# Kernel tuning notes

Hardware: AMD Instinct MI355X
Metric: run time of the kernel (lower is better)

Reference implementation:

```python
import jax, jax.numpy as jnp
import numpy as np

GRID = 128  # voxel grid extent
N_PTS = 100000


def _hash(c):
    c = c.astype(np.int64) + 16  # shift so offset-perturbed coords stay non-negative
    return (c[:, 0] * 512 + c[:, 1]) * 512 + c[:, 2]


def _offsets(vals):
    v = np.asarray(vals)
    return np.stack(np.meshgrid(v, v, v, indexing='ij'), axis=-1).reshape(-1, 3)


def _build_kmap(cin, cout, offsets):
    # For each kernel offset o, find pairs (in_idx, out_idx) with coord_in == coord_out + o.
    ki = _hash(cin)
    order = np.argsort(ki)
    ks = ki[order]
    ins, outs = [], []
    for o in offsets:
        q = _hash(cout + o[None, :])
        pos = np.searchsorted(ks, q)
        pc = np.clip(pos, 0, len(ks) - 1)
        found = ks[pc] == q
        ins.append(order[pc[found]])
        outs.append(np.nonzero(found)[0])
    K = len(offsets)
    P = max(1, max(len(a) for a in ins))
    in_idx = np.full((K, P), len(cin), np.int32)   # pad -> zero row of padded feats
    out_idx = np.full((K, P), len(cout), np.int32)  # pad -> dummy output row
    for k in range(K):
        in_idx[k, :len(ins[k])] = ins[k]
        out_idx[k, :len(outs[k])] = outs[k]
    return in_idx, out_idx


def _conv(x, W, in_idx, out_idx, n_out):
    # Minkowski sparse conv: per kernel offset, gather -> matmul -> scatter-add.
    xp = jnp.concatenate([x, jnp.zeros((1, x.shape[1]), x.dtype)], axis=0)
    out0 = jnp.zeros((n_out + 1, W.shape[-1]), x.dtype)

    def step(acc, kio):
        Wk, ik, ok = kio
        return acc.at[ok].add(xp[ik] @ Wk), None

    out, _ = jax.lax.scan(step, out0, (W, in_idx, out_idx))
    return out[:n_out]


def _bn(x, gamma, beta, eps=1e-5):
    # training-mode batch norm over the point dimension (biased variance)
    m = jnp.mean(x, axis=0)
    v = jnp.mean((x - m) ** 2, axis=0)
    return (x - m) * jax.lax.rsqrt(v + eps) * gamma + beta


def _forward(feats, W0, g0, b0,
             Ws1, gs1, bs1, Wa1, ga1, ba1, Wb1, gb1, bb1,
             Ws2, gs2, bs2, Wa2, ga2, ba2, Wb2, gb2, bb2, Wd2, gd2, bd2,
             Ws3, gs3, bs3, Wa3, ga3, ba3, Wb3, gb3, bb3, Wd3, gd3, bd3,
             c1, c2, c3,
             im0, om0, ims1, oms1, imb1, omb1, ims2, oms2, imb2, omb2,
             ims3, oms3, imb3, omb3):
    relu = jax.nn.relu
    n0, n1, n2, n3 = feats.shape[0], c1.shape[0], c2.shape[0], c3.shape[0]
    # stem: 5x5x5 conv + BN + ReLU (output coords == input coords)
    x = relu(_bn(_conv(feats, W0, im0, om0, n0), g0, b0))
    # level 1: stride-2 conv + BN + ReLU, then BasicBlock 64->64 (identity residual)
    x = relu(_bn(_conv(x, Ws1, ims1, oms1, n1), gs1, bs1))
    h = relu(_bn(_conv(x, Wa1, imb1, omb1, n1), ga1, ba1))
    h = _bn(_conv(h, Wb1, imb1, omb1, n1), gb1, bb1)
    y1 = relu(h + x)
    # level 2: stride-2 conv, then BasicBlock 64->128 (1x1 conv + BN residual)
    x = relu(_bn(_conv(y1, Ws2, ims2, oms2, n2), gs2, bs2))
    res = _bn(x @ Wd2, gd2, bd2)
    h = relu(_bn(_conv(x, Wa2, imb2, omb2, n2), ga2, ba2))
    h = _bn(_conv(h, Wb2, imb2, omb2, n2), gb2, bb2)
    y2 = relu(h + res)
    # level 3: stride-2 conv, then BasicBlock 128->256 (1x1 conv + BN residual)
    x = relu(_bn(_conv(y2, Ws3, ims3, oms3, n3), gs3, bs3))
    res = _bn(x @ Wd3, gd3, bd3)
    h = relu(_bn(_conv(x, Wa3, imb3, omb3, n3), ga3, ba3))
    h = _bn(_conv(h, Wb3, imb3, omb3, n3), gb3, bb3)
    y3 = relu(h + res)
    return (y1, y2, y3)


def setup_inputs() -> dict:
    rng = np.random.default_rng(0)
    c0 = np.unique(rng.integers(0, GRID, size=(N_PTS, 3)), axis=0).astype(np.int32)
    c1 = np.unique(c0 // 2 * 2, axis=0)
    c2 = np.unique(c1 // 4 * 4, axis=0)
    c3 = np.unique(c2 // 8 * 8, axis=0)
    im0, om0 = _build_kmap(c0, c0, _offsets([-2, -1, 0, 1, 2]))  # conv0 k=5, ts=1
    ims1, oms1 = _build_kmap(c0, c1, _offsets([0, 1]))           # stride-2, ts_in=1
    imb1, omb1 = _build_kmap(c1, c1, _offsets([-2, 0, 2]))       # k=3 at ts=2
    ims2, oms2 = _build_kmap(c1, c2, _offsets([0, 2]))
    imb2, omb2 = _build_kmap(c2, c2, _offsets([-4, 0, 4]))       # k=3 at ts=4
    ims3, oms3 = _build_kmap(c2, c3, _offsets([0, 4]))
    imb3, omb3 = _build_kmap(c3, c3, _offsets([-8, 0, 8]))       # k=3 at ts=8
    keys = iter(jax.random.split(jax.random.key(0), 16))

    def kai3(K, ci, co):  # kaiming_normal fan_out for [K, Cin, Cout] sparse kernels
        return jax.random.normal(next(keys), (K, ci, co), jnp.float32) * np.float32(np.sqrt(2.0 / (K * co)))

    def kai2(ci, co):
        return jax.random.normal(next(keys), (ci, co), jnp.float32) * np.float32(np.sqrt(2.0 / co))

    ones = lambda c: jnp.ones((c,), jnp.float32)
    zeros = lambda c: jnp.zeros((c,), jnp.float32)
    feats = jax.random.normal(next(keys), (c0.shape[0], 1), jnp.float32)
    return dict(
        feats=feats,
        W0=kai3(125, 1, 64), g0=ones(64), b0=zeros(64),
        Ws1=kai3(8, 64, 64), gs1=ones(64), bs1=zeros(64),
        Wa1=kai3(27, 64, 64), ga1=ones(64), ba1=zeros(64),
        Wb1=kai3(27, 64, 64), gb1=ones(64), bb1=zeros(64),
        Ws2=kai3(8, 64, 64), gs2=ones(64), bs2=zeros(64),
        Wa2=kai3(27, 64, 128), ga2=ones(128), ba2=zeros(128),
        Wb2=kai3(27, 128, 128), gb2=ones(128), bb2=zeros(128),
        Wd2=kai2(64, 128), gd2=ones(128), bd2=zeros(128),
        Ws3=kai3(8, 128, 128), gs3=ones(128), bs3=zeros(128),
        Wa3=kai3(27, 128, 256), ga3=ones(256), ba3=zeros(256),
        Wb3=kai3(27, 256, 256), gb3=ones(256), bb3=zeros(256),
        Wd3=kai2(128, 256), gd3=ones(256), bd3=zeros(256),
        c1=jnp.asarray(c1), c2=jnp.asarray(c2), c3=jnp.asarray(c3),
        im0=jnp.asarray(im0), om0=jnp.asarray(om0),
        ims1=jnp.asarray(ims1), oms1=jnp.asarray(oms1),
        imb1=jnp.asarray(imb1), omb1=jnp.asarray(omb1),
        ims2=jnp.asarray(ims2), oms2=jnp.asarray(oms2),
        imb2=jnp.asarray(imb2), omb2=jnp.asarray(omb2),
        ims3=jnp.asarray(ims3), oms3=jnp.asarray(oms3),
        imb3=jnp.asarray(imb3), omb3=jnp.asarray(omb3),
    )


def reference(feats, W0, g0, b0,
              Ws1, gs1, bs1, Wa1, ga1, ba1, Wb1, gb1, bb1,
              Ws2, gs2, bs2, Wa2, ga2, ba2, Wb2, gb2, bb2, Wd2, gd2, bd2,
              Ws3, gs3, bs3, Wa3, ga3, ba3, Wb3, gb3, bb3, Wd3, gd3, bd3,
              c1, c2, c3,
              im0, om0, ims1, oms1, imb1, omb1, ims2, oms2, imb2, omb2,
              ims3, oms3, imb3, omb3):
    return _forward(feats, W0, g0, b0,
                    Ws1, gs1, bs1, Wa1, ga1, ba1, Wb1, gb1, bb1,
                    Ws2, gs2, bs2, Wa2, ga2, ba2, Wb2, gb2, bb2, Wd2, gd2, bd2,
                    Ws3, gs3, bs3, Wa3, ga3, ba3, Wb3, gb3, bb3, Wd3, gd3, bd3,
                    c1, c2, c3,
                    im0, om0, ims1, oms1, imb1, omb1, ims2, oms2, imb2, omb2,
                    ims3, oms3, imb3, omb3)
```

## Files before the change

kernel.cpp:

```cpp
#include <hip/hip_runtime.h>
#include <hip/hip_bf16.h>
#include <cstdint>
#include <cstddef>

typedef __attribute__((ext_vector_type(8))) short sh8;
typedef __attribute__((ext_vector_type(4))) short sh4;
typedef __attribute__((ext_vector_type(4))) int ix4;
typedef __attribute__((ext_vector_type(16))) float floatx16;
typedef unsigned short ushort_t;

__device__ __forceinline__ void glds16(const ushort_t* g, ushort_t* l) {
  __builtin_amdgcn_global_load_lds(
      (const __attribute__((address_space(1))) void*)g,
      (__attribute__((address_space(3))) void*)l, 16, 0, 0);
}

__device__ __forceinline__ ushort_t f2bf_bits(float f) {
  __hip_bfloat16 b = __float2bfloat16(f);
  return __builtin_bit_cast(unsigned short, b);
}
__device__ __forceinline__ float bf2f(ushort_t u) {
  unsigned int x = ((unsigned int)u) << 16;
  return __builtin_bit_cast(float, x);
}

__global__ void build_ell_kernel(const int* __restrict__ in_idx,
                                 const int* __restrict__ out_idx,
                                 int K, int S, int P, int n_in, int n_out,
                                 int* __restrict__ ell) {
  int i = blockIdx.x * 256 + threadIdx.x;
  if (i >= K * P) return;
  int vin = in_idx[i];
  int vout = out_idx[i];
  if (vin < n_in && vout < n_out) {
    ell[(size_t)vout * S + (i / P)] = vin;
  }
}

__global__ void pack_u_kernel(const float* __restrict__ W,
                              __hip_bfloat16* __restrict__ Wp,
                              int K, int CSPLIT, int COUT, long total) {
  long i = (long)blockIdx.x * 256 + threadIdx.x;
  if (i >= total) return;
  int co = (int)(i % COUT);
  long t = i / COUT;
  int vch = (int)(t % 64);
  int vk = (int)(t / 64);
  int k = vk / CSPLIT;
  int ci = (vk % CSPLIT) * 64 + vch;
  int CIN = CSPLIT * 64;
  float v = (k < K) ? W[((long)k * CIN + ci) * COUT + co] : 0.f;
  Wp[(((long)vk * 8 + (vch >> 3)) * COUT + co) * 8 + (vch & 7)] =
      __float2bfloat16(v);
}

__global__ void pack_w0_kernel(const float* __restrict__ W,
                               __hip_bfloat16* __restrict__ Wp) {
  int i = blockIdx.x * 256 + threadIdx.x;
  if (i >= 128 * 64) return;
  int co = i & 63;
  int ki = i >> 6;
  float v = (ki < 125) ? W[ki * 64 + co] : 0.f;
  Wp[(((ki >> 4) * 64) + co) * 16 + (ki & 15)] = __float2bfloat16(v);
}

__global__ void f2bf_kernel(const float* __restrict__ x,
                            __hip_bfloat16* __restrict__ y, long n, long npad) {
  long i = (long)blockIdx.x * 256 + threadIdx.x;
  if (i >= npad) return;
  y[i] = __float2bfloat16(i < n ? x[i] : 0.f);
}

__global__ void reduce_parts_kernel(const ushort_t* __restrict__ part, int P,
                                    long total, ushort_t* __restrict__ out) {
  long i = (long)blockIdx.x * 256 + threadIdx.x;
  if (i >= total) return;
  float s = 0.f;
  for (int p = 0; p < P; ++p) s += bf2f(part[(size_t)p * total + i]);
  out[i] = f2bf_bits(s);
}

__global__ __launch_bounds__(256, 2) void conv0_mfma_kernel(
    const ushort_t* __restrict__ xpad, const ushort_t* __restrict__ Wp0,
    const int* __restrict__ ell, int n_out, ushort_t* __restrict__ out) {
  constexpr int STR = 152;
  __shared__ ushort_t xs[64 * STR];
  const int tid = threadIdx.x;
  const int lane = tid & 63;
  const int wv = tid >> 6;
  const int wm = wv & 1, wn = wv >> 1;
  const long m0 = (long)blockIdx.x * 64;
  const int row = tid >> 2;
  const int kk0 = (tid & 3) * 32;
  const long grow = m0 + row;

  if (grow < n_out) {
    const ix4* ep = (const ix4*)(ell + grow * 128 + kk0);
#pragma unroll
    for (int g = 0; g < 8; ++g) {
      ix4 e = ep[g];
      sh4 v;
#pragma unroll
      for (int j = 0; j < 4; ++j) {
        int ix = (e[j] < 0) ? n_out : e[j];
        v[j] = (short)xpad[ix];
      }
      *(sh4*)(&xs[row * STR + kk0 + g * 4]) = v;
    }
  } else {
    sh4 z = (sh4)(short)0;
#pragma unroll
    for (int g = 0; g < 8; ++g) *(sh4*)(&xs[row * STR + kk0 + g * 4]) = z;
  }
  __syncthreads();

  const int arow = wm * 32 + (lane & 31);
  const int koff = (lane >> 5) * 8;
  const int bcol = wn * 32 + (lane & 31);
  floatx16 acc = (floatx16)(0.0f);
#pragma unroll
  for (int kc = 0; kc < 8; ++kc) {
    sh8 a = *(const sh8*)(&xs[arow * STR + kc * 16 + koff]);
    sh8 b = *(const sh8*)(Wp0 + ((size_t)kc * 64 + bcol) * 16 + koff);
    acc = __builtin_amdgcn_mfma_f32_32x32x16_bf16(a, b, acc, 0, 0, 0);
  }
  const int lrow = (lane >> 5) * 4;
#pragma unroll
  for (int r = 0; r < 16; ++r) {
    long orow = m0 + wm * 32 + (r & 3) + 8 * (r >> 2) + lrow;
    if (orow < n_out) out[orow * 64 + bcol] = f2bf_bits(acc[r]);
  }
}

template <int CSPLIT, int CT, bool HASELL>
__global__ __launch_bounds__(CT * 4, CT == 128 ? 4 : 3) void conv_u_kernel(
    const ushort_t* __restrict__ xb, const ushort_t* __restrict__ Wp,
    const int* __restrict__ ell, int S, int KI, int KP, int kdense,
    int n_out, int n_in, int COfull, int MB, int KS, int CS,
    ushort_t* __restrict__ out) {
  constexpr int BLK = CT * 4;
  constexpr int NWN = CT / 32;
  constexpr int ASEG_PW = 16 / (BLK / 64);
  constexpr int BSEG_PW = (CT / 8) / (BLK / 64);
  constexpr int RW = CSPLIT * 64;
  __shared__ ushort_t Ab[2][128 * 64];
  __shared__ ushort_t Bb[2][8 * CT * 8];
  const int tid = threadIdx.x;
  const int lane = tid & 63;
  const int wv = tid >> 6;
  const int wm = wv / NWN, wn = wv % NWN;

  const int total = MB * KS * CS;
  const int l = blockIdx.x;
  const int q = total >> 3, r8 = total & 7;
  const int xcd = l & 7, pos = l >> 3;
  const int lp = (xcd < r8) ? (xcd * (q + 1) + pos)
                            : (r8 * (q + 1) + (xcd - r8) * q + pos);
  const int mblk = lp / (KS * CS);
  const int rem = lp - mblk * (KS * CS);
  const int yk = rem / CS;
  const int zc = rem - yk * CS;
  const long m0 = (long)mblk * 128;
  const int colbase = zc * CT;

  const int i0 = yk * KP;
  int cnt = KI - i0;
  if (cnt > KP) cnt = KP;
  out += (size_t)yk * ((size_t)n_out * COfull);

  floatx16 acc0 = (floatx16)(0.0f);
  floatx16 acc1 = (floatx16)(0.0f);

  auto loadEll = [&](int vk, int (&e)[ASEG_PW]) {
    if constexpr (HASELL) {
      const int kq = (CSPLIT == 1) ? vk : (vk / CSPLIT);
#pragma unroll
      for (int i = 0; i < ASEG_PW; ++i) {
        const int s = wv * ASEG_PW + i;
        const int r = s * 8 + (lane >> 3);
        long grow = m0 + r;
        long gc = grow < (long)(n_out - 1) ? grow : (long)(n_out - 1);
        e[i] = ell[gc * (long)S + kq];
      }
    }
  };

  auto stage = [&](int vk, ushort_t* A, ushort_t* B, int (&eRaw)[ASEG_PW]) {
    const int sub = (CSPLIT == 1) ? 0 : (vk % CSPLIT);
    const int kq = (CSPLIT == 1) ? vk : (vk / CSPLIT);
#pragma unroll
    for (int i = 0; i < ASEG_PW; ++i) {
      const int s = wv * ASEG_PW + i;
      const int r = s * 8 + (lane >> 3);
      const long grow = m0 + r;
      int v;
      if constexpr (HASELL) v = eRaw[i];
      else v = (kq < kdense) ? (int)grow : -1;
      if (grow >= (long)n_out) v = -1;
      const int e = (v < 0) ? n_in : v;
      const int c = lane & 7;
      const int lc = c ^ (r & 7);
      glds16(xb + (size_t)e * RW + sub * 64 + lc * 8, A + s * 512 + lane * 8);
    }
    const ushort_t* wb = Wp + (size_t)vk * 8 * COfull * 8;
#pragma unroll
    for (int i = 0; i < BSEG_PW; ++i) {
      const int s = wv * BSEG_PW + i;
      int lc, co;
      if (CT == 128) { lc = s >> 1; co = (s & 1) * 64 + lane; }
      else           { lc = s;      co = lane; }
      glds16(wb + ((size_t)lc * COfull + colbase + co) * 8,
             B + s * 512 + lane * 8);
    }
  };
  auto compute = [&](const ushort_t* A, const ushort_t* B) {
    const int r0 = wm * 64 + (lane & 31);
    const int h = lane >> 5;
    const int co = wn * 32 + (lane & 31);
#pragma unroll
    for (int kc = 0; kc < 4; ++kc) {
      const int lc = kc * 2 + h;
      const int pc = lc ^ (r0 & 7);
      sh8 a0 = *(const sh8*)(A + r0 * 64 + pc * 8);
      sh8 a1 = *(const sh8*)(A + (r0 + 32) * 64 + pc * 8);
      sh8 b = *(const sh8*)(B + ((size_t)lc * CT + co) * 8);
      acc0 = __builtin_amdgcn_mfma_f32_32x32x16_bf16(a0, b, acc0, 0, 0, 0);
      acc1 = __builtin_amdgcn_mfma_f32_32x32x16_bf16(a1, b, acc1, 0, 0, 0);
    }
  };

  constexpr int NWAIT = (ASEG_PW + BSEG_PW) + (HASELL ? ASEG_PW : 0);

  int eE[ASEG_PW] = {}, eO[ASEG_PW] = {};
  loadEll(i0, eE);
  stage(i0, Ab[0], Bb[0], eE);
  if (cnt > 1) loadEll(i0 + 1, eO);

#define CONV_ITER(J, P, SE, SO)                                                \
  if ((J) < cnt) {                                                             \
    __builtin_amdgcn_sched_barrier(0);             \
    asm volatile("s_waitcnt lgkmcnt(0)" ::: "memory");                         \
    __builtin_amdgcn_s_barrier();        \
    if ((J) + 1 < cnt) {                                                       \
      stage(i0 + (J) + 1, Ab[(P) ^ 1], Bb[(P) ^ 1], SO);                       \
      if ((J) + 2 < cnt) loadEll(i0 + (J) + 2, SE);                            \
      if constexpr (NWAIT == 4)                                                \
        asm volatile("s_waitcnt vmcnt(4)" ::: "memory");                       \
      else if constexpr (NWAIT == 6)                                           \
        asm volatile("s_waitcnt vmcnt(6)" ::: "memory");                       \
      else                                                                     \
        asm volatile("s_waitcnt vmcnt(10)" ::: "memory");                      \
    } else {                                                                   \
      asm volatile("s_waitcnt vmcnt(0)" ::: "memory");                         \
    }                                                                          \
    __builtin_amdgcn_s_barrier();           \
    __builtin_amdgcn_sched_barrier(0);                                         \
    compute(Ab[P], Bb[P]);                                                     \
  }

  for (int j = 0; j < cnt; j += 2) {
    CONV_ITER(j, 0, eE, eO)
    CONV_ITER(j + 1, 1, eO, eE)
  }
#undef CONV_ITER

  const int ccol = colbase + wn * 32 + (lane & 31);
  const int rb = wm * 64 + (lane >> 5) * 4;
#pragma unroll
  for (int rr = 0; rr < 16; ++rr) {
    long row = m0 + rb + (rr & 3) + 8 * (rr >> 2);
    if (row < n_out) out[row * COfull + ccol] = f2bf_bits(acc0[rr]);
    long row1 = row + 32;
    if (row1 < n_out) out[row1 * COfull + ccol] = f2bf_bits(acc1[rr]);
  }
}

template <int C>
__global__ void bn_reduce1_kernel(const ushort_t* __restrict__ x, int n,
                                  float* __restrict__ part) {
  constexpr int C4 = C / 4;
  constexpr int RL = 256 / C4;
  const int c4 = threadIdx.x % C4;
  const int rl = threadIdx.x / C4;
  float4 s = {0.f, 0.f, 0.f, 0.f}, ss = {0.f, 0.f, 0.f, 0.f};
  for (long row = (long)blockIdx.x * RL + rl; row < n;
       row += (long)gridDim.x * RL) {
    ushort4 u = *(const ushort4*)(x + row * C + c4 * 4);
    float v0 = bf2f(u.x), v1 = bf2f(u.y), v2 = bf2f(u.z), v3 = bf2f(u.w);
    s.x += v0; s.y += v1; s.z += v2; s.w += v3;
    ss.x += v0 * v0; ss.y += v1 * v1; ss.z += v2 * v2; ss.w += v3 * v3;
  }
  __shared__ float4 sh[512];
  sh[threadIdx.x] = s;
  sh[256 + threadIdx.x] = ss;
  __syncthreads();
  if (rl == 0) {
#pragma unroll
    for (int j = 1; j < RL; ++j) {
      float4 a = sh[j * C4 + c4];
      float4 b = sh[256 + j * C4 + c4];
      s.x += a.x; s.y += a.y; s.z += a.z; s.w += a.w;
      ss.x += b.x; ss.y += b.y; ss.z += b.z; ss.w += b.w;
    }
    *(float4*)(part + (size_t)blockIdx.x * 2 * C + c4 * 4) = s;
    *(float4*)(part + (size_t)blockIdx.x * 2 * C + C + c4 * 4) = ss;
  }
}

template <int C>
__global__ void bn_reduce2_kernel(const float* __restrict__ part, int G,
                                  float* __restrict__ stats) {
  const int c = blockIdx.x;
  const int g = threadIdx.x;
  __shared__ float sh[512];
  float s = 0.f, ss = 0.f;
  if (g < G) {
    s = part[(size_t)g * 2 * C + c];
    ss = part[(size_t)g * 2 * C + C + c];
  }
  sh[g] = s;
  sh[256 + g] = ss;
  __syncthreads();
#pragma unroll
  for (int off = 128; off > 0; off >>= 1) {
    if (g < off) {
      sh[g] += sh[g + off];
      sh[256 + g] += sh[256 + g + off];
    }
    __syncthreads();
  }
  if (g == 0) {
    stats[c] = sh[0];
    stats[C + c] = sh[256];
  }
}

template <int C, bool RELU, bool RES, bool WF32>
__global__ void bn_apply_kernel(const ushort_t* __restrict__ x,
                                const float* __restrict__ stats,
                                const float* __restrict__ gamma,
                                const float* __restrict__ beta,
                                const float* __restrict__ res,
                                long total4, float inv_n,
                                float* __restrict__ out,
                                ushort_t* __restrict__ outb, long padEnd4) {
  constexpr int C4 = C / 4;
  for (long i = (long)blockIdx.x * 256 + threadIdx.x; i < padEnd4;
       i += (long)gridDim.x * 256) {
    if (i >= total4) {
      if (outb) *(ushort4*)(outb + i * 4) = (ushort4){0, 0, 0, 0};
      continue;
    }
    const int c4 = (int)(i % C4);
    float4 sum = *(const float4*)(stats + c4 * 4);
    float4 sq = *(const float4*)(stats + C + c4 * 4);
    float4 g4 = *(const float4*)(gamma + c4 * 4);
    float4 b4 = *(const float4*)(beta + c4 * 4);
    ushort4 u = *(const ushort4*)(x + i * 4);
    float vin[4] = {bf2f(u.x), bf2f(u.y), bf2f(u.z), bf2f(u.w)};
    float4 r4 = {0.f, 0.f, 0.f, 0.f};
    if (RES) r4 = *(const float4*)(res + i * 4);
    float o[4];
#pragma unroll
    for (int j = 0; j < 4; ++j) {
      float m = ((const float*)&sum)[j] * inv_n;
      float var = ((const float*)&sq)[j] * inv_n - m * m;
      float sc = rsqrtf(var + 1e-5f) * ((const float*)&g4)[j];
      float val = (vin[j] - m) * sc + ((const float*)&b4)[j];
      if (RES) val += ((const float*)&r4)[j];
      if (RELU) val = fmaxf(val, 0.f);
      o[j] = val;
    }
    if (WF32) *(float4*)(out + i * 4) = (float4){o[0], o[1], o[2], o[3]};
    if (outb) {
      ushort4 w = {f2bf_bits(o[0]), f2bf_bits(o[1]), f2bf_bits(o[2]),
                   f2bf_bits(o[3])};
      *(ushort4*)(outb + i * 4) = w;
    }
  }
}


extern "C" void kernel_launch(void* const* d_in, const int* in_sizes, int n_in,
                              void* d_out, int out_size, void* d_ws,
                              size_t ws_size, hipStream_t stream) {
  const float* feats = (const float*)d_in[0];
  const float* W0  = (const float*)d_in[1];
  const float* g0  = (const float*)d_in[2];
  const float* b0  = (const float*)d_in[3];
  const float* Ws1 = (const float*)d_in[4];
  const float* gs1 = (const float*)d_in[5];
  const float* bs1 = (const float*)d_in[6];
  const float* Wa1 = (const float*)d_in[7];
  const float* ga1 = (const float*)d_in[8];
  const float* ba1 = (const float*)d_in[9];
  const float* Wb1 = (const float*)d_in[10];
  const float* gb1 = (const float*)d_in[11];
  const float* bb1 = (const float*)d_in[12];
  const float* Ws2 = (const float*)d_in[13];
  const float* gs2 = (const float*)d_in[14];
  const float* bs2 = (const float*)d_in[15];
  const float* Wa2 = (const float*)d_in[16];
  const float* ga2 = (const float*)d_in[17];
  const float* ba2 = (const float*)d_in[18];
  const float* Wb2 = (const float*)d_in[19];
  const float* gb2 = (const float*)d_in[20];
  const float* bb2 = (const float*)d_in[21];
  const float* Wd2 = (const float*)d_in[22];
  const float* gd2 = (const float*)d_in[23];
  const float* bd2 = (const float*)d_in[24];
  const float* Ws3 = (const float*)d_in[25];
  const float* gs3 = (const float*)d_in[26];
  const float* bs3 = (const float*)d_in[27];
  const float* Wa3 = (const float*)d_in[28];
  const float* ga3 = (const float*)d_in[29];
  const float* ba3 = (const float*)d_in[30];
  const float* Wb3 = (const float*)d_in[31];
  const float* gb3 = (const float*)d_in[32];
  const float* bb3 = (const float*)d_in[33];
  const float* Wd3 = (const float*)d_in[34];
  const float* gd3 = (const float*)d_in[35];
  const float* bd3 = (const float*)d_in[36];
  const int* im0  = (const int*)d_in[40];
  const int* om0  = (const int*)d_in[41];
  const int* ims1 = (const int*)d_in[42];
  const int* oms1 = (const int*)d_in[43];
  const int* imb1 = (const int*)d_in[44];
  const int* omb1 = (const int*)d_in[45];
  const int* ims2 = (const int*)d_in[46];
  const int* oms2 = (const int*)d_in[47];
  const int* imb2 = (const int*)d_in[48];
  const int* omb2 = (const int*)d_in[49];
  const int* ims3 = (const int*)d_in[50];
  const int* oms3 = (const int*)d_in[51];
  const int* imb3 = (const int*)d_in[52];
  const int* omb3 = (const int*)d_in[53];

  const int n0 = in_sizes[0];
  const int n1 = in_sizes[37] / 3;
  const int n2 = in_sizes[38] / 3;
  const int n3 = in_sizes[39] / 3;
  const int P0  = in_sizes[40] / 125;
  const int Ps1 = in_sizes[42] / 8;
  const int Pb1 = in_sizes[44] / 27;
  const int Ps2 = in_sizes[46] / 8;
  const int Pb2 = in_sizes[48] / 27;
  const int Ps3 = in_sizes[50] / 8;
  const int Pb3 = in_sizes[52] / 27;

  char* w = (char*)d_ws;
  auto carve = [&](size_t bytes) {
    char* p = w;
    w += (bytes + 255) & ~(size_t)255;
    return p;
  };
  int* ellS = (int*)carve((size_t)n0 * 128 * sizeof(int));
  int* ellB = (int*)carve((size_t)n1 * 28 * sizeof(int));
  float* part = (float*)carve((size_t)256 * 512 * sizeof(float));
  float* stats = (float*)carve((size_t)512 * sizeof(float));
  size_t capE = (size_t)n0 * 64 + 512;
  float* buf1 = (float*)carve(capE * sizeof(float));
  float* buf2 = (float*)carve(capE * sizeof(float));
  __hip_bfloat16* bbA = (__hip_bfloat16*)carve(capE * 2);
  __hip_bfloat16* bbB = (__hip_bfloat16*)carve(capE * 2);
  __hip_bfloat16* bbC = (__hip_bfloat16*)carve(capE * 2);
  ushort_t* cb1 = (ushort_t*)carve(capE * 2);
  ushort_t* cb2 = (ushort_t*)carve(capE * 2);
  ushort_t* cb3 = (ushort_t*)carve(capE * 2);
  __hip_bfloat16* xfeat = (__hip_bfloat16*)carve(((size_t)n0 + 1) * 2);

  auto packu = [&](const float* W, int K, int cin, int cout) {
    int csplit = cin / 64;
    long tot = (long)K * csplit * 64 * cout;
    __hip_bfloat16* Wp = (__hip_bfloat16*)carve((size_t)tot * 2);
    pack_u_kernel<<<(int)((tot + 255) / 256), 256, 0, stream>>>(
        W, Wp, K, csplit, cout, tot);
    return Wp;
  };
  __hip_bfloat16* Wp0 = (__hip_bfloat16*)carve((size_t)128 * 64 * 2);
  pack_w0_kernel<<<32, 256, 0, stream>>>(W0, Wp0);
  __hip_bfloat16* Ps1p = packu(Ws1, 8, 64, 64);
  __hip_bfloat16* Pa1p = packu(Wa1, 27, 64, 64);
  __hip_bfloat16* Pb1p = packu(Wb1, 27, 64, 64);
  __hip_bfloat16* Ps2p = packu(Ws2, 8, 64, 64);
  __hip_bfloat16* Pd2p = packu(Wd2, 1, 64, 128);
  __hip_bfloat16* Pa2p = packu(Wa2, 27, 64, 128);
  __hip_bfloat16* Pb2p = packu(Wb2, 27, 128, 128);
  __hip_bfloat16* Ps3p = packu(Ws3, 8, 128, 128);
  __hip_bfloat16* Pd3p = packu(Wd3, 1, 128, 256);
  __hip_bfloat16* Pa3p = packu(Wa3, 27, 128, 256);
  __hip_bfloat16* Pb3p = packu(Wb3, 27, 256, 256);

  size_t used = (size_t)(w - (char*)d_ws);
  ushort_t* pbufU = (ushort_t*)w;
  size_t pcapU = (ws_size > used) ? (ws_size - used) / 2 : 0;

  f2bf_kernel<<<(int)((n0 + 256) / 256), 256, 0, stream>>>(feats, xfeat, n0,
                                                           n0 + 1);

  auto buildEll = [&](int* ellbuf, const int* im, const int* om, int K, int S,
                      int P, int nin, int nout) {
    hipMemsetAsync(ellbuf, 0xFF, (size_t)nout * S * sizeof(int), stream);
    int tot = K * P;
    build_ell_kernel<<<(tot + 255) / 256, 256, 0, stream>>>(im, om, K, S, P,
                                                            nin, nout, ellbuf);
  };

  auto convu = [&](const __hip_bfloat16* xb, const __hip_bfloat16* Wp,
                   const int* ellp, int S, int K, int kdense, int nout,
                   int nin, int cin, int cout, ushort_t* outc) {
    int csplit = cin / 64;
    int KIv = K * csplit;
    int CT = (cout >= 128) ? 128 : 64;
    int cs = cout / CT;
    int mb = (nout + 127) / 128;
    int tiles = mb * cs;
    int ks = 1;
    if (tiles < 512 && KIv > 1) {
      ks = (512 + tiles - 1) / tiles;
      if (ks > 8) ks = 8;
      if (ks > KIv) ks = KIv;
      size_t need = (size_t)nout * cout;
      int fit = need ? (int)(pcapU / need) : 1;
      if (ks > fit) ks = fit;
      if (ks < 1) ks = 1;
    }
    int KP = (KIv + ks - 1) / ks;
    int ksE = (KIv + KP - 1) / KP;
    ushort_t* tgt = (ksE > 1) ? pbufU : outc;
    int gridx = mb * ksE * cs;
#define CU_CASE(CSV, CTV)                                                      \
  else if (csplit == CSV && CT == CTV) {                                       \
    if (ellp)                                                                  \
      conv_u_kernel<CSV, CTV, true><<<gridx, CTV * 4, 0, stream>>>(            \
          (const ushort_t*)xb, (const ushort_t*)Wp, ellp, S, KIv, KP, kdense,  \
          nout, nin, cout, mb, ksE, cs, tgt);                                  \
    else                                                                       \
      conv_u_kernel<CSV, CTV, false><<<gridx, CTV * 4, 0, stream>>>(           \
          (const ushort_t*)xb, (const ushort_t*)Wp, ellp, S, KIv, KP, kdense,  \
          nout, nin, cout, mb, ksE, cs, tgt);                                  \
  }
    if (false) {}
    CU_CASE(1, 64)
    CU_CASE(1, 128)
    CU_CASE(2, 128)
    CU_CASE(4, 128)
#undef CU_CASE
    if (ksE > 1) {
      long total = (long)nout * cout;
      reduce_parts_kernel<<<(int)((total + 255) / 256), 256, 0, stream>>>(
          pbufU, ksE, total, outc);
    }
  };

  auto bn = [&](const ushort_t* x, int n, int C, const float* gamma,
                const float* beta, const float* res, bool relu, float* outp,
                __hip_bfloat16* outb) {
    const int G = 256;
    float invn = 1.0f / (float)n;
    long total4 = (long)n * C / 4;
    long padEnd4 = outb ? (total4 + C / 4) : total4;
    int agrid = (int)((padEnd4 + 255) / 256);
    if (agrid > 2048) agrid = 2048;
    ushort_t* outbu = (ushort_t*)outb;
#define BN_CASE(CC)                                                            \
  else if (C == CC) {                                                          \
    bn_reduce1_kernel<CC><<<G, 256, 0, stream>>>(x, n, part);                  \
    bn_reduce2_kernel<CC><<<CC, 256, 0, stream>>>(part, G, stats);             \
    if (res && relu)                                                           \
      bn_apply_kernel<CC, true, true, true><<<agrid, 256, 0, stream>>>(        \
          x, stats, gamma, beta, res, total4, invn, outp, outbu, padEnd4);     \
    else if (relu && outp)                                                     \
      bn_apply_kernel<CC, true, false, true><<<agrid, 256, 0, stream>>>(       \
          x, stats, gamma, beta, nullptr, total4, invn, outp, outbu,           \
          padEnd4);                                                            \
    else if (relu)                                                             \
      bn_apply_kernel<CC, true, false, false><<<agrid, 256, 0, stream>>>(      \
          x, stats, gamma, beta, nullptr, total4, invn, nullptr, outbu,        \
          padEnd4);                                                            \
    else                                                                       \
      bn_apply_kernel<CC, false, false, true><<<agrid, 256, 0, stream>>>(      \
          x, stats, gamma, beta, nullptr, total4, invn, outp, outbu,           \
          padEnd4);                                                            \
  }
    if (false) {}
    BN_CASE(64)
    BN_CASE(128)
    BN_CASE(256)
#undef BN_CASE
  };

  float* y1 = (float*)d_out;
  float* y2 = y1 + (size_t)n1 * 64;
  float* y3 = y2 + (size_t)n2 * 128;

  buildEll(ellS, im0, om0, 125, 128, P0, n0, n0);
  conv0_mfma_kernel<<<(n0 + 63) / 64, 256, 0, stream>>>(
      (const ushort_t*)xfeat, (const ushort_t*)Wp0, ellS, n0, cb1);
  bn(cb1, n0, 64, g0, b0, nullptr, true, nullptr, bbA);

  buildEll(ellS, ims1, oms1, 8, 8, Ps1, n0, n1);
  convu(bbA, Ps1p, ellS, 8, 8, 0, n1, n0, 64, 64, cb2);
  bn(cb2, n1, 64, gs1, bs1, nullptr, true, buf2, bbB);
  buildEll(ellB, imb1, omb1, 27, 28, Pb1, n1, n1);
  convu(bbB, Pa1p, ellB, 28, 27, 0, n1, n1, 64, 64, cb3);
  bn(cb3, n1, 64, ga1, ba1, nullptr, true, nullptr, bbC);
  convu(bbC, Pb1p, ellB, 28, 27, 0, n1, n1, 64, 64, cb1);
  bn(cb1, n1, 64, gb1, bb1, buf2, true, y1, bbA);

  buildEll(ellS, ims2, oms2, 8, 8, Ps2, n1, n2);
  convu(bbA, Ps2p, ellS, 8, 8, 0, n2, n1, 64, 64, cb2);
  bn(cb2, n2, 64, gs2, bs2, nullptr, true, nullptr, bbB);
  convu(bbB, Pd2p, nullptr, 1, 1, 1, n2, n2, 64, 128, cb3);
  bn(cb3, n2, 128, gd2, bd2, nullptr, false, buf1, nullptr);
  buildEll(ellB, imb2, omb2, 27, 28, Pb2, n2, n2);
  convu(bbB, Pa2p, ellB, 28, 27, 0, n2, n2, 64, 128, cb2);
  bn(cb2, n2, 128, ga2, ba2, nullptr, true, nullptr, bbC);
  convu(bbC, Pb2p, ellB, 28, 27, 0, n2, n2, 128, 128, cb3);
  bn(cb3, n2, 128, gb2, bb2, buf1, true, y2, bbA);

  buildEll(ellS, ims3, oms3, 8, 8, Ps3, n2, n3);
  convu(bbA, Ps3p, ellS, 8, 8, 0, n3, n2, 128, 128, cb1);
  bn(cb1, n3, 128, gs3, bs3, nullptr, true, nullptr, bbB);
  convu(bbB, Pd3p, nullptr, 1, 1, 1, n3, n3, 128, 256, cb2);
  bn(cb2, n3, 256, gd3, bd3, nullptr, false, buf2, nullptr);
  buildEll(ellB, imb3, omb3, 27, 28, Pb3, n3, n3);
  convu(bbB, Pa3p, ellB, 28, 27, 0, n3, n3, 128, 256, cb1);
  bn(cb1, n3, 256, ga3, ba3, nullptr, true, nullptr, bbC);
  convu(bbC, Pb3p, ellB, 28, 27, 0, n3, n3, 256, 256, cb2);
  bn(cb2, n3, 256, gb3, bb3, buf2, true, y3, nullptr);
}
```

Before: 617.9 us.

## Batch weight packing and ELL builds, fuse split-K reduction with BN statistics

The eleven per-layer weight-packing launches become one kernel driven by a descriptor table. The two ELL map builds per level, each with its own memset, become one init kernel plus one combined build kernel. The split-K partial-sum reduction now also writes per-block BN sum and sum-of-squares, so BN skips its separate first reduction pass. The aim is fewer kernel launches and one less full read of the conv output, at the cost of more complex kernels and a descriptor search per thread during packing.

```diff
diff --git a/kernel.cpp b/kernel.cpp
--- a/kernel.cpp
+++ b/kernel.cpp
@@ -22,6 +22,30 @@
 __device__ __forceinline__ float bf2f(ushort_t u) {
   unsigned int x = ((unsigned int)u) << 16;
   return __builtin_bit_cast(float, x);
+}
+
+__global__ void init_ell2_kernel(int* __restrict__ e1, long sz1,
+                                 int* __restrict__ e2, long sz2) {
+  long i = (long)blockIdx.x * 256 + threadIdx.x;
+  if (i < sz1) e1[i] = -1;
+  else if (i < sz1 + sz2) e2[i - sz1] = -1;
+}
+
+__global__ void build_ell2_kernel(
+    const int* __restrict__ i1, const int* __restrict__ o1, int K1, int S1,
+    int P1, int nin1, int nout1, int* __restrict__ e1,
+    const int* __restrict__ i2, const int* __restrict__ o2, int K2, int S2,
+    int P2, int nin2, int nout2, int* __restrict__ e2) {
+  long i = (long)blockIdx.x * 256 + threadIdx.x;
+  long t1 = (long)K1 * P1;
+  if (i < t1) {
+    int vin = i1[i], vout = o1[i];
+    if (vin < nin1 && vout < nout1) e1[(size_t)vout * S1 + (i / P1)] = vin;
+  } else if (i < t1 + (long)K2 * P2) {
+    long j = i - t1;
+    int vin = i2[j], vout = o2[j];
+    if (vin < nin2 && vout < nout2) e2[(size_t)vout * S2 + (j / P2)] = vin;
+  }
 }
 
 __global__ void build_ell_kernel(const int* __restrict__ in_idx,
@@ -37,21 +61,35 @@
   }
 }
 
-__global__ void pack_u_kernel(const float* __restrict__ W,
-                              __hip_bfloat16* __restrict__ Wp,
-                              int K, int CSPLIT, int COUT, long total) {
+struct PackDesc {
+  const float* W;
+  ushort_t* Wp;
+  int K, CSPLIT, COUT, pad;
+};
+struct PackAll {
+  PackDesc d[11];
+  long cum[12];
+};
+
+__global__ void pack_all_kernel(PackAll pa, long grand) {
   long i = (long)blockIdx.x * 256 + threadIdx.x;
-  if (i >= total) return;
-  int co = (int)(i % COUT);
-  long t = i / COUT;
+  if (i >= grand) return;
+  int di = 0;
+#pragma unroll
+  for (int s = 0; s < 11; ++s)
+    if (i >= pa.cum[s + 1]) di = s + 1;
+  const PackDesc& D = pa.d[di];
+  long j = i - pa.cum[di];
+  int co = (int)(j % D.COUT);
+  long t = j / D.COUT;
   int vch = (int)(t % 64);
   int vk = (int)(t / 64);
-  int k = vk / CSPLIT;
-  int ci = (vk % CSPLIT) * 64 + vch;
-  int CIN = CSPLIT * 64;
-  float v = (k < K) ? W[((long)k * CIN + ci) * COUT + co] : 0.f;
-  Wp[(((long)vk * 8 + (vch >> 3)) * COUT + co) * 8 + (vch & 7)] =
-      __float2bfloat16(v);
+  int k = vk / D.CSPLIT;
+  int ci = (vk % D.CSPLIT) * 64 + vch;
+  int CIN = D.CSPLIT * 64;
+  float v = (k < D.K) ? D.W[((long)k * CIN + ci) * D.COUT + co] : 0.f;
+  D.Wp[(((long)vk * 8 + (vch >> 3)) * D.COUT + co) * 8 + (vch & 7)] =
+      f2bf_bits(v);
 }
 
 __global__ void pack_w0_kernel(const float* __restrict__ W,
@@ -78,6 +116,48 @@
   float s = 0.f;
   for (int p = 0; p < P; ++p) s += bf2f(part[(size_t)p * total + i]);
   out[i] = f2bf_bits(s);
+}
+
+template <int C>
+__global__ void reduce_parts_stats_kernel(const ushort_t* __restrict__ pin,
+                                          int P, int n,
+                                          ushort_t* __restrict__ out,
+                                          float* __restrict__ part) {
+  constexpr int C4 = C / 4;
+  constexpr int RL = 256 / C4;
+  const long total = (long)n * C;
+  const int c4 = threadIdx.x % C4;
+  const int rl = threadIdx.x / C4;
+  float4 s = {0.f, 0.f, 0.f, 0.f}, ss = {0.f, 0.f, 0.f, 0.f};
+  for (long row = (long)blockIdx.x * RL + rl; row < n;
+       row += (long)gridDim.x * RL) {
+    long base = row * C + c4 * 4;
+    float f0 = 0.f, f1 = 0.f, f2 = 0.f, f3 = 0.f;
+    for (int p = 0; p < P; ++p) {
+      ushort4 u = *(const ushort4*)(pin + (size_t)p * total + base);
+      f0 += bf2f(u.x); f1 += bf2f(u.y); f2 += bf2f(u.z); f3 += bf2f(u.w);
+    }
+    ushort4 w = {f2bf_bits(f0), f2bf_bits(f1), f2bf_bits(f2), f2bf_bits(f3)};
+    *(ushort4*)(out + base) = w;
+    float v0 = bf2f(w.x), v1 = bf2f(w.y), v2 = bf2f(w.z), v3 = bf2f(w.w);
+    s.x += v0; s.y += v1; s.z += v2; s.w += v3;
+    ss.x += v0 * v0; ss.y += v1 * v1; ss.z += v2 * v2; ss.w += v3 * v3;
+  }
+  __shared__ float4 sh[512];
+  sh[threadIdx.x] = s;
+  sh[256 + threadIdx.x] = ss;
+  __syncthreads();
+  if (rl == 0) {
+#pragma unroll
+    for (int j = 1; j < RL; ++j) {
+      float4 a = sh[j * C4 + c4];
+      float4 b = sh[256 + j * C4 + c4];
+      s.x += a.x; s.y += a.y; s.z += a.z; s.w += a.w;
+      ss.x += b.x; ss.y += b.y; ss.z += b.z; ss.w += b.w;
+    }
+    *(float4*)(part + (size_t)blockIdx.x * 2 * C + c4 * 4) = s;
+    *(float4*)(part + (size_t)blockIdx.x * 2 * C + C + c4 * 4) = ss;
+  }
 }
 
 __global__ __launch_bounds__(256, 2) void conv0_mfma_kernel(
@@ -469,27 +549,33 @@
   ushort_t* cb3 = (ushort_t*)carve(capE * 2);
   __hip_bfloat16* xfeat = (__hip_bfloat16*)carve(((size_t)n0 + 1) * 2);
 
-  auto packu = [&](const float* W, int K, int cin, int cout) {
+  PackAll pa;
+  long cum = 0;
+  auto addPack = [&](int idx, const float* W, int K, int cin, int cout) {
     int csplit = cin / 64;
-    long tot = (long)K * csplit * 64 * cout;
-    __hip_bfloat16* Wp = (__hip_bfloat16*)carve((size_t)tot * 2);
-    pack_u_kernel<<<(int)((tot + 255) / 256), 256, 0, stream>>>(
-        W, Wp, K, csplit, cout, tot);
+    long elems = (long)K * csplit * 64 * cout;
+    ushort_t* Wp = (ushort_t*)carve((size_t)elems * 2);
+    pa.d[idx] = {W, Wp, K, csplit, cout, 0};
+    pa.cum[idx] = cum;
+    cum += elems;
     return Wp;
   };
+  ushort_t* Ps1p = addPack(0, Ws1, 8, 64, 64);
+  ushort_t* Pa1p = addPack(1, Wa1, 27, 64, 64);
+  ushort_t* Pb1p = addPack(2, Wb1, 27, 64, 64);
+  ushort_t* Ps2p = addPack(3, Ws2, 8, 64, 64);
+  ushort_t* Pd2p = addPack(4, Wd2, 1, 64, 128);
+  ushort_t* Pa2p = addPack(5, Wa2, 27, 64, 128);
+  ushort_t* Pb2p = addPack(6, Wb2, 27, 128, 128);
+  ushort_t* Ps3p = addPack(7, Ws3, 8, 128, 128);
+  ushort_t* Pd3p = addPack(8, Wd3, 1, 128, 256);
+  ushort_t* Pa3p = addPack(9, Wa3, 27, 128, 256);
+  ushort_t* Pb3p = addPack(10, Wb3, 27, 256, 256);
+  pa.cum[11] = cum;
   __hip_bfloat16* Wp0 = (__hip_bfloat16*)carve((size_t)128 * 64 * 2);
+
+  pack_all_kernel<<<(int)((cum + 255) / 256), 256, 0, stream>>>(pa, cum);
   pack_w0_kernel<<<32, 256, 0, stream>>>(W0, Wp0);
-  __hip_bfloat16* Ps1p = packu(Ws1, 8, 64, 64);
-  __hip_bfloat16* Pa1p = packu(Wa1, 27, 64, 64);
-  __hip_bfloat16* Pb1p = packu(Wb1, 27, 64, 64);
-  __hip_bfloat16* Ps2p = packu(Ws2, 8, 64, 64);
-  __hip_bfloat16* Pd2p = packu(Wd2, 1, 64, 128);
-  __hip_bfloat16* Pa2p = packu(Wa2, 27, 64, 128);
-  __hip_bfloat16* Pb2p = packu(Wb2, 27, 128, 128);
-  __hip_bfloat16* Ps3p = packu(Ws3, 8, 128, 128);
-  __hip_bfloat16* Pd3p = packu(Wd3, 1, 128, 256);
-  __hip_bfloat16* Pa3p = packu(Wa3, 27, 128, 256);
-  __hip_bfloat16* Pb3p = packu(Wb3, 27, 256, 256);
 
   size_t used = (size_t)(w - (char*)d_ws);
   ushort_t* pbufU = (ushort_t*)w;
@@ -498,17 +584,21 @@
   f2bf_kernel<<<(int)((n0 + 256) / 256), 256, 0, stream>>>(feats, xfeat, n0,
                                                            n0 + 1);
 
-  auto buildEll = [&](int* ellbuf, const int* im, const int* om, int K, int S,
-                      int P, int nin, int nout) {
-    hipMemsetAsync(ellbuf, 0xFF, (size_t)nout * S * sizeof(int), stream);
-    int tot = K * P;
-    build_ell_kernel<<<(tot + 255) / 256, 256, 0, stream>>>(im, om, K, S, P,
-                                                            nin, nout, ellbuf);
+  auto buildLevel = [&](const int* ims, const int* oms, int Ps, int nin_s,
+                        int nout_s, const int* imb, const int* omb, int Pb,
+                        int n_b) {
+    long sz1 = (long)nout_s * 8, sz2 = (long)n_b * 28;
+    init_ell2_kernel<<<(int)((sz1 + sz2 + 255) / 256), 256, 0, stream>>>(
+        ellS, sz1, ellB, sz2);
+    long t = (long)8 * Ps + (long)27 * Pb;
+    build_ell2_kernel<<<(int)((t + 255) / 256), 256, 0, stream>>>(
+        ims, oms, 8, 8, Ps, nin_s, nout_s, ellS,
+        imb, omb, 27, 28, Pb, n_b, n_b, ellB);
   };
 
-  auto convu = [&](const __hip_bfloat16* xb, const __hip_bfloat16* Wp,
-                   const int* ellp, int S, int K, int kdense, int nout,
-                   int nin, int cin, int cout, ushort_t* outc) {
+  auto convu = [&](const void* xb, const ushort_t* Wp, const int* ellp, int S,
+                   int K, int kdense, int nout, int nin, int cin, int cout,
+                   ushort_t* outc) -> bool {
     int csplit = cin / 64;
     int KIv = K * csplit;
     int CT = (cout >= 128) ? 128 : 64;
@@ -533,12 +623,12 @@
   else if (csplit == CSV && CT == CTV) {                                       \
     if (ellp)                                                                  \
       conv_u_kernel<CSV, CTV, true><<<gridx, CTV * 4, 0, stream>>>(            \
-          (const ushort_t*)xb, (const ushort_t*)Wp, ellp, S, KIv, KP, kdense,  \
-          nout, nin, cout, mb, ksE, cs, tgt);                                  \
+          (const ushort_t*)xb, Wp, ellp, S, KIv, KP, kdense, nout, nin, cout,  \
+          mb, ksE, cs, tgt);                                                   \
     else                                                                       \
       conv_u_kernel<CSV, CTV, false><<<gridx, CTV * 4, 0, stream>>>(           \
-          (const ushort_t*)xb, (const ushort_t*)Wp, ellp, S, KIv, KP, kdense,  \
-          nout, nin, cout, mb, ksE, cs, tgt);                                  \
+          (const ushort_t*)xb, Wp, ellp, S, KIv, KP, kdense, nout, nin, cout,  \
+          mb, ksE, cs, tgt);                                                   \
   }
     if (false) {}
     CU_CASE(1, 64)
@@ -547,15 +637,26 @@
     CU_CASE(4, 128)
 #undef CU_CASE
     if (ksE > 1) {
-      long total = (long)nout * cout;
-      reduce_parts_kernel<<<(int)((total + 255) / 256), 256, 0, stream>>>(
-          pbufU, ksE, total, outc);
-    }
+      if (cout == 64)
+        reduce_parts_stats_kernel<64><<<256, 256, 0, stream>>>(pbufU, ksE,
+                                                               nout, outc,
+                                                               part);
+      else if (cout == 128)
+        reduce_parts_stats_kernel<128><<<256, 256, 0, stream>>>(pbufU, ksE,
+                                                                nout, outc,
+                                                                part);
+      else
+        reduce_parts_stats_kernel<256><<<256, 256, 0, stream>>>(pbufU, ksE,
+                                                                nout, outc,
+                                                                part);
+      return true;
+    }
+    return false;
   };
 
   auto bn = [&](const ushort_t* x, int n, int C, const float* gamma,
                 const float* beta, const float* res, bool relu, float* outp,
-                __hip_bfloat16* outb) {
+                __hip_bfloat16* outb, bool haveStats) {
     const int G = 256;
     float invn = 1.0f / (float)n;
     long total4 = (long)n * C / 4;
@@ -565,7 +666,8 @@
     ushort_t* outbu = (ushort_t*)outb;
 #define BN_CASE(CC)                                                            \
   else if (C == CC) {                                                          \
-    bn_reduce1_kernel<CC><<<G, 256, 0, stream>>>(x, n, part);                  \
+    if (!haveStats)                                                            \
+      bn_reduce1_kernel<CC><<<G, 256, 0, stream>>>(x, n, part);                \
     bn_reduce2_kernel<CC><<<CC, 256, 0, stream>>>(part, G, stats);             \
     if (res && relu)                                                           \
       bn_apply_kernel<CC, true, true, true><<<agrid, 256, 0, stream>>>(        \
@@ -594,39 +696,42 @@
   float* y2 = y1 + (size_t)n1 * 64;
   float* y3 = y2 + (size_t)n2 * 128;
 
-  buildEll(ellS, im0, om0, 125, 128, P0, n0, n0);
-  conv0_mfma_kernel<<<(n0 + 63) / 64, 256, 0, stream>>>(
-      (const ushort_t*)xfeat, (const ushort_t*)Wp0, ellS, n0, cb1);
-  bn(cb1, n0, 64, g0, b0, nullptr, true, nullptr, bbA);
-
-  buildEll(ellS, ims1, oms1, 8, 8, Ps1, n0, n1);
-  convu(bbA, Ps1p, ellS, 8, 8, 0, n1, n0, 64, 64, cb2);
-  bn(cb2, n1, 64, gs1, bs1, nullptr, true, buf2, bbB);
-  buildEll(ellB, imb1, omb1, 27, 28, Pb1, n1, n1);
-  convu(bbB, Pa1p, ellB, 28, 27, 0, n1, n1, 64, 64, cb3);
-  bn(cb3, n1, 64, ga1, ba1, nullptr, true, nullptr, bbC);
-  convu(bbC, Pb1p, ellB, 28, 27, 0, n1, n1, 64, 64, cb1);
-  bn(cb1, n1, 64, gb1, bb1, buf2, true, y1, bbA);
-
-  buildEll(ellS, ims2, oms2, 8, 8, Ps2, n1, n2);
-  convu(bbA, Ps2p, ellS, 8, 8, 0, n2, n1, 64, 64, cb2);
-  bn(cb2, n2, 64, gs2, bs2, nullptr, true, nullptr, bbB);
-  convu(bbB, Pd2p, nullptr, 1, 1, 1, n2, n2, 64, 128, cb3);
-  bn(cb3, n2, 128, gd2, bd2, nullptr, false, buf1, nullptr);
-  buildEll(ellB, imb2, omb2, 27, 28, Pb2, n2, n2);
-  convu(bbB, Pa2p, ellB, 28, 27, 0, n2, n2, 64, 128, cb2);
-  bn(cb2, n2, 128, ga2, ba2, nullptr, true, nullptr, bbC);
-  convu(bbC, Pb2p, ellB, 28, 27, 0, n2, n2, 128, 128, cb3);
-  bn(cb3, n2, 128, gb2, bb2, buf1, true, y2, bbA);
-
-  buildEll(ellS, ims3, oms3, 8, 8, Ps3, n2, n3);
-  convu(bbA, Ps3p, ellS, 8, 8, 0, n3, n2, 128, 128, cb1);
-  bn(cb1, n3, 128, gs3, bs3, nullptr, true, nullptr, bbB);
-  convu(bbB, Pd3p, nullptr, 1, 1, 1, n3, n3, 128, 256, cb2);
-  bn(cb2, n3, 256, gd3, bd3, nullptr, false, buf2, nullptr);
-  buildEll(ellB, imb3, omb3, 27, 28, Pb3, n3, n3);
-  convu(bbB, Pa3p, ellB, 28, 27, 0, n3, n3, 128, 256, cb1);
-  bn(cb1, n3, 256, ga3, ba3, nullptr, true, nullptr, bbC);
-  convu(bbC, Pb3p, ellB, 28, 27, 0, n3, n3, 256, 256, cb2);
-  bn(cb2, n3, 256, gb3, bb3, buf2, true, y3, nullptr);
-}
+  {
+    hipMemsetAsync(ellS, 0xFF, (size_t)n0 * 128 * sizeof(int), stream);
+    int tot = 125 * P0;
+    build_ell_kernel<<<(tot + 255) / 256, 256, 0, stream>>>(im0, om0, 125, 128,
+                                                            P0, n0, n0, ellS);
+    conv0_mfma_kernel<<<(n0 + 63) / 64, 256, 0, stream>>>(
+        (const ushort_t*)xfeat, (const ushort_t*)Wp0, ellS, n0, cb1);
+  }
+  bn(cb1, n0, 64, g0, b0, nullptr, true, nullptr, bbA, false);
+
+  buildLevel(ims1, oms1, Ps1, n0, n1, imb1, omb1, Pb1, n1);
+  bool st;
+  st = convu(bbA, Ps1p, ellS, 8, 8, 0, n1, n0, 64, 64, cb2);
+  bn(cb2, n1, 64, gs1, bs1, nullptr, true, buf2, bbB, st);
+  st = convu(bbB, Pa1p, ellB, 28, 27, 0, n1, n1, 64, 64, cb3);
+  bn(cb3, n1, 64, ga1, ba1, nullptr, true, nullptr, bbC, st);
+  st = convu(bbC, Pb1p, ellB, 28, 27, 0, n1, n1, 64, 64, cb1);
+  bn(cb1, n1, 64, gb1, bb1, buf2, true, y1, bbA, st);
+
+  buildLevel(ims2, oms2, Ps2, n1, n2, imb2, omb2, Pb2, n2);
+  st = convu(bbA, Ps2p, ellS, 8, 8, 0, n2, n1, 64, 64, cb2);
+  bn(cb2, n2, 64, gs2, bs2, nullptr, true, nullptr, bbB, st);
+  st = convu(bbB, Pd2p, nullptr, 1, 1, 1, n2, n2, 64, 128, cb3);
+  bn(cb3, n2, 128, gd2, bd2, nullptr, false, buf1, nullptr, st);
+  st = convu(bbB, Pa2p, ellB, 28, 27, 0, n2, n2, 64, 128, cb2);
+  bn(cb2, n2, 128, ga2, ba2, nullptr, true, nullptr, bbC, st);
+  st = convu(bbC, Pb2p, ellB, 28, 27, 0, n2, n2, 128, 128, cb3);
+  bn(cb3, n2, 128, gb2, bb2, buf1, true, y2, bbA, st);
+
+  buildLevel(ims3, oms3, Ps3, n2, n3, imb3, omb3, Pb3, n3);
+  st = convu(bbA, Ps3p, ellS, 8, 8, 0, n3, n2, 128, 128, cb1);
+  bn(cb1, n3, 128, gs3, bs3, nullptr, true, nullptr, bbB, st);
+  st = convu(bbB, Pd3p, nullptr, 1, 1, 1, n3, n3, 128, 256, cb2);
+  bn(cb2, n3, 256, gd3, bd3, nullptr, false, buf2, nullptr, st);
+  st = convu(bbB, Pa3p, ellB, 28, 27, 0, n3, n3, 128, 256, cb1);
+  bn(cb1, n3, 256, ga3, ba3, nullptr, true, nullptr, bbC, st);
+  st = convu(bbC, Pb3p, ellB, 28, 27, 0, n3, n3, 256, 256, cb2);
+  bn(cb2, n3, 256, gb3, bb3, buf2, true, y3, nullptr, st);
+}
```

After: 599.2 us, median of 2. -3.0%, faster.
